# Kernel optimization log

Hardware: AMD Instinct MI355X
Metric: run time of the kernel (lower is better)

The kernel has to match this reference:

```python
import jax, jax.numpy as jnp
import numpy as np
import math

B, S, D, H, DF, L = 8, 1024, 1024, 16, 4096, 2
DK = D // H

def cosine_pe(seq_len, d_model):
    pos = jnp.arange(seq_len, dtype=jnp.float32)[:, None]
    div = jnp.exp(jnp.arange(0, d_model, 2, dtype=jnp.float32) * (-math.log(10000.0) / d_model))
    ang = pos * div[None, :]  # [S, D/2]
    # interleave sin (even cols) and cos (odd cols)
    return jnp.stack([jnp.sin(ang), jnp.cos(ang)], axis=-1).reshape(seq_len, d_model)

def layernorm(x, g, b, eps=1e-5):
    m = jnp.mean(x, axis=-1, keepdims=True)
    v = jnp.mean((x - m) ** 2, axis=-1, keepdims=True)
    return (x - m) / jnp.sqrt(v + eps) * g + b

def setup_inputs() -> dict:
    key = jax.random.key(0)
    ks = jax.random.split(key, 8)
    w = 0.03  # ~xavier scale for d_model=1024
    return {
        "q_embed_data": jax.random.normal(ks[0], (B, S, D), dtype=jnp.float32),
        "qa_embed_data": jax.random.normal(ks[1], (B, S, D), dtype=jnp.float32),
        "Wk": jax.random.normal(ks[2], (L, D, D), dtype=jnp.float32) * w,
        "bk": jnp.zeros((L, D), jnp.float32),
        "Wv": jax.random.normal(ks[3], (L, D, D), dtype=jnp.float32) * w,
        "bv": jnp.zeros((L, D), jnp.float32),
        "Wo": jax.random.normal(ks[4], (L, D, D), dtype=jnp.float32) * w,
        "bo": jnp.zeros((L, D), jnp.float32),
        "ln1_g": jnp.ones((L, D), jnp.float32),
        "ln1_b": jnp.zeros((L, D), jnp.float32),
        "W1": jax.random.normal(ks[5], (L, DF, D), dtype=jnp.float32) * w,
        "b1": jnp.zeros((L, DF), jnp.float32),
        "W2": jax.random.normal(ks[6], (L, D, DF), dtype=jnp.float32) * w,
        "b2": jnp.zeros((L, D), jnp.float32),
        "ln2_g": jnp.ones((L, D), jnp.float32),
        "ln2_b": jnp.zeros((L, D), jnp.float32),
    }

def reference(q_embed_data, qa_embed_data, Wk, bk, Wv, bv, Wo, bo, ln1_g, ln1_b, W1, b1, W2, b2, ln2_g, ln2_b):
    b, s, d = q_embed_data.shape
    pe = cosine_pe(s, d)
    x = q_embed_data + pe[None]   # query/key stream, updated per block
    y = qa_embed_data + pe[None]  # value stream, fixed across blocks
    idx = jnp.arange(s)
    allow = idx[None, :] < idx[:, None]  # strict causal: only past (j < i)
    n_blocks = Wk.shape[0]
    for l in range(n_blocks):
        # kq_same=True: q and k share k_linear
        q = (x @ Wk[l].T + bk[l]).reshape(b, s, H, DK).transpose(0, 2, 1, 3)
        k = q  # same input and same projection
        v = (y @ Wv[l].T + bv[l]).reshape(b, s, H, DK).transpose(0, 2, 1, 3)
        scores = jnp.einsum('bhid,bhjd->bhij', q, k) / math.sqrt(DK)
        scores = jnp.where(allow[None, None], scores, jnp.float32(-1e32))
        p = jax.nn.softmax(scores, axis=-1)
        p = p.at[:, :, 0, :].set(0.0)  # zero_pad first query row
        attn = jnp.einsum('bhij,bhjd->bhid', p, v).transpose(0, 2, 1, 3).reshape(b, s, d)
        attn = attn @ Wo[l].T + bo[l]
        x = layernorm(x + attn, ln1_g[l], ln1_b[l])
        ff = jax.nn.relu(x @ W1[l].T + b1[l]) @ W2[l].T + b2[l]
        x = layernorm(x + ff, ln2_g[l], ln2_b[l])
    return x
```

## Files before the change

### kernel.cpp

```cpp
#include <hip/hip_runtime.h>

using bf16   = __bf16;
using bf16x4 = __attribute__((ext_vector_type(4))) __bf16;
using bf16x8 = __attribute__((ext_vector_type(8))) __bf16;
using f32x4  = __attribute__((ext_vector_type(4))) float;

#define GLDS16(g, l)                                                            \
  __builtin_amdgcn_global_load_lds(                                             \
      (__attribute__((address_space(1))) void*)(g),                             \
      (__attribute__((address_space(3))) void*)(l), 16, 0, 0)

#define MFMA16(a, b, c) __builtin_amdgcn_mfma_f32_16x16x32_bf16(a, b, c, 0, 0, 0)

__device__ __forceinline__ int SW(int r, int s) {
  return r * 64 + (((s ^ (r & 7) ^ ((r >> 3) & 7)) & 7) << 3);
}

__device__ __forceinline__ float b2f(unsigned short u) {
  return (float)__builtin_bit_cast(bf16, u);
}

__device__ __forceinline__ bf16x8 scale8th(bf16x8 v) {
  bf16x8 r;
#pragma unroll
  for (int i = 0; i < 8; ++i) r[i] = (bf16)((float)v[i] * 0.125f);
  return r;
}

__global__ __launch_bounds__(256)
void init_pe(const float4* __restrict__ qd, const float4* __restrict__ qa,
             ushort4* __restrict__ xbf, ushort4* __restrict__ ybf) {
  const int n4 = 8 * 1024 * 1024 / 4;
  for (int i = blockIdx.x * 256 + threadIdx.x; i < n4; i += gridDim.x * 256) {
    int d4 = (i & 255) * 4;
    int ss = (i >> 8) & 1023;
    const float c = -0.0089944730195177f;
    float a0 = (float)ss * __expf((float)d4 * c);
    float a1 = (float)ss * __expf((float)(d4 + 2) * c);
    float p0 = sinf(a0), p1 = cosf(a0), p2 = sinf(a1), p3 = cosf(a1);
    float4 q4 = qd[i], y4 = qa[i];
    ushort4 xb, yb;
    xb.x = __builtin_bit_cast(unsigned short, (bf16)(q4.x + p0));
    xb.y = __builtin_bit_cast(unsigned short, (bf16)(q4.y + p1));
    xb.z = __builtin_bit_cast(unsigned short, (bf16)(q4.z + p2));
    xb.w = __builtin_bit_cast(unsigned short, (bf16)(q4.w + p3));
    yb.x = __builtin_bit_cast(unsigned short, (bf16)(y4.x + p0));
    yb.y = __builtin_bit_cast(unsigned short, (bf16)(y4.y + p1));
    yb.z = __builtin_bit_cast(unsigned short, (bf16)(y4.z + p2));
    yb.w = __builtin_bit_cast(unsigned short, (bf16)(y4.w + p3));
    xbf[i] = xb; ybf[i] = yb;
  }
}

__global__ __launch_bounds__(256)
void cvt5(const float4* __restrict__ s0, const float4* __restrict__ s1,
          const float4* __restrict__ s2, const float4* __restrict__ s3,
          const float4* __restrict__ s4,
          ushort4* __restrict__ dDD, ushort4* __restrict__ dDF,
          int n4dd, int n4df) {
  const int z = blockIdx.z;
  const float4* s = (z == 0) ? s0 : (z == 1) ? s1 : (z == 2) ? s2 : (z == 3) ? s3 : s4;
  ushort4* dd = (z < 3) ? dDD + (size_t)z * n4dd : dDF + (size_t)(z - 3) * n4df;
  const int n4 = (z < 3) ? n4dd : n4df;
  for (int i = blockIdx.x * 256 + threadIdx.x; i < n4; i += gridDim.x * 256) {
    float4 v = s[i];
    ushort4 o;
    o.x = __builtin_bit_cast(unsigned short, (bf16)v.x);
    o.y = __builtin_bit_cast(unsigned short, (bf16)v.y);
    o.z = __builtin_bit_cast(unsigned short, (bf16)v.z);
    o.w = __builtin_bit_cast(unsigned short, (bf16)v.w);
    dd[i] = o;
  }
}

template <int EPI, int MODE>
__global__ __launch_bounds__(256, 4)
void gemm_s(const bf16* __restrict__ A0, const bf16* __restrict__ W0,
            const float* __restrict__ b0, void* __restrict__ C0,
            const bf16* __restrict__ A1, const bf16* __restrict__ W1,
            const float* __restrict__ b1, void* __restrict__ C1,
            const int N, const int K) {
  __shared__ bf16 L[2][128 * 64];

  const int tid = threadIdx.x;
  const int wave = tid >> 6, lane = tid & 63;
  const int wm = wave >> 1, wn = wave & 1;
  const int cl = lane & 15, hk = lane >> 4;

  const int gx = gridDim.x;
  int flat = blockIdx.y * gx + blockIdx.x;
  flat = (flat & 7) * ((gx * gridDim.y) >> 3) + (flat >> 3);
  const int bcol = flat % gx, brow = flat / gx;
  const int z = (MODE == 0) ? 0 : blockIdx.z;

  const bf16* A = (MODE == 1 && z) ? A1 : A0;
  const bf16* W = (MODE == 1 && z) ? W1 : W0;
  const float* bias = (MODE == 1 && z) ? b1 : b0;
  void* C = (MODE == 1 && z) ? C1 : C0;

  const bf16* Ablk = A + (size_t)brow * 128 * K;
  const bf16* Wblk = W + (size_t)bcol * 128 * K;

  const int strow8 = lane >> 3;
  const int sl8 = (lane & 7) ^ (lane >> 3);

#define STAGE(kt)                                                               \
  do {                                                                          \
    _Pragma("unroll") for (int i_ = 0; i_ < 4; ++i_) {                          \
      int r0_ = i_ * 32 + wave * 8;                                             \
      GLDS16(Ablk + (size_t)(r0_ + strow8) * K + (size_t)(kt) * 64 + sl8 * 8,   \
             &L[0][r0_ * 64]);                                                  \
      GLDS16(Wblk + (size_t)(r0_ + strow8) * K + (size_t)(kt) * 64 + sl8 * 8,   \
             &L[1][r0_ * 64]);                                                  \
    }                                                                           \
  } while (0)

#define RD(reg, r_, kk_) \
  (*(const bf16x8*)&L[reg][(r_) * 64 + ((((kk_) * 4 + hk) ^ (cl & 7)) * 8)])

  f32x4 acc[4][4] = {};
  const int NT = K >> 6;

  for (int t = 0; t < NT; ++t) {
    STAGE(t);
    __syncthreads();
#pragma unroll
    for (int kk = 0; kk < 2; ++kk) {
      bf16x8 a4[4], b4[4];
#pragma unroll
      for (int m = 0; m < 4; ++m) a4[m] = RD(0, wm * 64 + m * 16 + cl, kk);
#pragma unroll
      for (int n = 0; n < 4; ++n) b4[n] = RD(1, wn * 64 + n * 16 + cl, kk);
      __builtin_amdgcn_s_setprio(1);
#pragma unroll
      for (int m = 0; m < 4; ++m)
#pragma unroll
        for (int n = 0; n < 4; ++n)
          acc[m][n] = MFMA16(a4[m], b4[n], acc[m][n]);
      __builtin_amdgcn_s_setprio(0);
    }
    __syncthreads();
  }
#undef STAGE
#undef RD

  float bv[4];
#pragma unroll
  for (int n = 0; n < 4; ++n)
    bv[n] = bias[bcol * 128 + wn * 64 + n * 16 + cl];

  const int crow0 = brow * 128 + wm * 64;
  const int ccol0 = bcol * 128 + wn * 64;
  char* esmem = (char*)(&L[0][0]) + wave * 4608;

  if (MODE == 1 && z == 1) {
    bf16* ep = (bf16*)esmem;
    const int h_ = ccol0 >> 6;
#pragma unroll
    for (int mp = 0; mp < 2; ++mp) {
#pragma unroll
      for (int mb = 0; mb < 2; ++mb) {
        int m = mp * 2 + mb;
#pragma unroll
        for (int n = 0; n < 4; ++n) {
          bf16x4 w4;
#pragma unroll
          for (int j = 0; j < 4; ++j) w4[j] = (bf16)(acc[m][n][j] + bv[n]);
          *(bf16x4*)&ep[(n * 16 + cl) * 36 + mb * 16 + hk * 4] = w4;
        }
      }
      asm volatile("s_waitcnt lgkmcnt(0)" ::: "memory");
      __builtin_amdgcn_sched_barrier(0);
      {
        const int t0 = crow0 + mp * 32;
        const int b_ = t0 >> 10, s_ = t0 & 1023;
        bf16* dst = (bf16*)C + ((size_t)(b_ * 16 + h_) * 64 + lane) * 1024 + s_;
        const bf16* src = &ep[lane * 36];
#pragma unroll
        for (int i = 0; i < 4; ++i)
          *(bf16x8*)&dst[i * 8] = *(const bf16x8*)&src[i * 8];
      }
      asm volatile("s_waitcnt lgkmcnt(0)" ::: "memory");
      __builtin_amdgcn_sched_barrier(0);
    }
  } else {
#pragma unroll
    for (int m = 0; m < 4; ++m) {
      bf16* ep = (bf16*)esmem;
#pragma unroll
      for (int n = 0; n < 4; ++n)
#pragma unroll
        for (int j = 0; j < 4; ++j) {
          float val = acc[m][n][j] + bv[n];
          if (EPI == 1) val = fmaxf(val, 0.f);
          ep[(hk * 4 + j) * 64 + n * 16 + cl] = (bf16)val;
        }
      asm volatile("s_waitcnt lgkmcnt(0)" ::: "memory");
      __builtin_amdgcn_sched_barrier(0);
#pragma unroll
      for (int i = 0; i < 2; ++i) {
        bf16x8 vv = ((const bf16x8*)ep)[lane + i * 64];
        const int row = crow0 + m * 16 + 8 * i + (lane >> 3);
        *(bf16x8*)((bf16*)C + (size_t)row * N + ccol0 + (lane & 7) * 8) = vv;
      }
      asm volatile("s_waitcnt lgkmcnt(0)" ::: "memory");
      __builtin_amdgcn_sched_barrier(0);
    }
  }
}

template <int EPI>
__global__ __launch_bounds__(512, 2)
void gemm8(const bf16* __restrict__ A, const bf16* __restrict__ W,
           const float* __restrict__ bias, bf16* __restrict__ C,
           const int N, const int K) {
  extern __shared__ bf16 lds[];

  const int tid = threadIdx.x;
  const int wave = tid >> 6, lane = tid & 63;
  const int wm = wave >> 2, wn = wave & 3;
  const int cl = lane & 15, hk = lane >> 4;
  const int sl8 = (lane & 7) ^ (lane >> 3);

  const int gx = gridDim.x;
  int flat = blockIdx.y * gx + blockIdx.x;
  flat = (flat & 7) * ((gx * gridDim.y) >> 3) + (flat >> 3);
  const int bcol = flat % gx, brow = flat / gx;

  const bf16* Ablk = A + (size_t)brow * 256 * K;
  const bf16* Wblk = W + (size_t)bcol * 256 * K;
  const size_t srow = (size_t)(wave * 8 + (lane >> 3)) * K + sl8 * 8;

  const int NT = K >> 6;

#define STG8(src, r0, dstbase, kt)                                             \
  do {                                                                         \
    _Pragma("unroll") for (int i_ = 0; i_ < 2; ++i_)                           \
      GLDS16((src) + srow + (size_t)((r0) + i_ * 64) * K + (size_t)(kt) * 64,  \
             (dstbase) + ((r0) + i_ * 64 + wave * 8) * 64);                    \
  } while (0)

#define RDF(base, r, kk) \
  (*(const bf16x8*)&(base)[(r) * 64 + ((((kk) * 4 + hk) ^ ((r) & 7)) * 8)])

#define BAR8 asm volatile("s_barrier" ::: "memory")

  STG8(Ablk, 0, lds, 0);
  STG8(Ablk, 128, lds, 0);
  STG8(Wblk, 0, lds + 16384, 0);
  STG8(Wblk, 128, lds + 16384, 0);
  STG8(Wblk, 0, lds + 49152, 1);
  STG8(Ablk, 0, lds + 32768, 1);
  asm volatile("s_waitcnt vmcnt(4)" ::: "memory");
  BAR8;

  f32x4 acc[2][2][4][2] = {};
  bf16x8 a[2][4], b0[2][2], b1[2][2];

  for (int t = 0; t < NT; ++t) {
    bf16* Ab = lds + (t & 1) * 32768;
    bf16* Bb = Ab + 16384;
    bf16* An = lds + (((t & 1) ^ 1)) * 32768;
    bf16* Bn = An + 16384;

#pragma unroll
    for (int kk = 0; kk < 2; ++kk) {
#pragma unroll
      for (int m_ = 0; m_ < 4; ++m_)
        a[kk][m_] = RDF(Ab, wm * 128 + m_ * 16 + cl, kk);
#pragma unroll
      for (int n_ = 0; n_ < 2; ++n_)
        b0[kk][n_] = RDF(Bb, wn * 64 + n_ * 16 + cl, kk);
    }
    if (t + 1 < NT) STG8(Ablk, 128, An, t + 1);
    BAR8;
    __builtin_amdgcn_s_setprio(1);
#pragma unroll
    for (int kk = 0; kk < 2; ++kk)
#pragma unroll
      for (int m_ = 0; m_ < 4; ++m_)
#pragma unroll
        for (int n_ = 0; n_ < 2; ++n_)
          acc[0][0][m_][n_] = MFMA16(a[kk][m_], b0[kk][n_], acc[0][0][m_][n_]);
    __builtin_amdgcn_s_setprio(0);
    BAR8;

#pragma unroll
    for (int kk = 0; kk < 2; ++kk)
#pragma unroll
      for (int n_ = 0; n_ < 2; ++n_)
        b1[kk][n_] = RDF(Bb, wn * 64 + 32 + n_ * 16 + cl, kk);
    if (t + 1 < NT) STG8(Wblk, 128, Bn, t + 1);
    BAR8;
    __builtin_amdgcn_s_setprio(1);
#pragma unroll
    for (int kk = 0; kk < 2; ++kk)
#pragma unroll
      for (int m_ = 0; m_ < 4; ++m_)
#pragma unroll
        for (int n_ = 0; n_ < 2; ++n_)
          acc[0][1][m_][n_] = MFMA16(a[kk][m_], b1[kk][n_], acc[0][1][m_][n_]);
    __builtin_amdgcn_s_setprio(0);
    BAR8;

#pragma unroll
    for (int kk = 0; kk < 2; ++kk)
#pragma unroll
      for (int m_ = 0; m_ < 4; ++m_)
        a[kk][m_] = RDF(Ab, wm * 128 + 64 + m_ * 16 + cl, kk);
    if (t + 2 < NT) STG8(Wblk, 0, Bb, t + 2);
    BAR8;
    __builtin_amdgcn_s_setprio(1);
#pragma unroll
    for (int kk = 0; kk < 2; ++kk)
#pragma unroll
      for (int m_ = 0; m_ < 4; ++m_)
#pragma unroll
        for (int n_ = 0; n_ < 2; ++n_)
          acc[1][0][m_][n_] = MFMA16(a[kk][m_], b0[kk][n_], acc[1][0][m_][n_]);
    __builtin_amdgcn_s_setprio(0);
    BAR8;

    if (t + 2 < NT) {
      STG8(Ablk, 0, Ab, t + 2);
      asm volatile("s_waitcnt vmcnt(4)" ::: "memory");
    } else if (t + 1 < NT) {
      asm volatile("s_waitcnt vmcnt(0)" ::: "memory");
    }
    BAR8;
    __builtin_amdgcn_s_setprio(1);
#pragma unroll
    for (int kk = 0; kk < 2; ++kk)
#pragma unroll
      for (int m_ = 0; m_ < 4; ++m_)
#pragma unroll
        for (int n_ = 0; n_ < 2; ++n_)
          acc[1][1][m_][n_] = MFMA16(a[kk][m_], b1[kk][n_], acc[1][1][m_][n_]);
    __builtin_amdgcn_s_setprio(0);
    BAR8;
  }
#undef STG8
#undef RDF
#undef BAR8

  __syncthreads();

  float bv[2][2];
#pragma unroll
  for (int nh = 0; nh < 2; ++nh)
#pragma unroll
    for (int n_ = 0; n_ < 2; ++n_)
      bv[nh][n_] = bias[bcol * 256 + wn * 64 + nh * 32 + n_ * 16 + cl];

  const int crow0 = brow * 256 + wm * 128;
  const int ccol0 = bcol * 256 + wn * 64;
  bf16* ep = lds + wave * 2304;

#pragma unroll
  for (int mh = 0; mh < 2; ++mh)
#pragma unroll
    for (int m_ = 0; m_ < 4; ++m_) {
#pragma unroll
      for (int nh = 0; nh < 2; ++nh)
#pragma unroll
        for (int n_ = 0; n_ < 2; ++n_)
#pragma unroll
          for (int j = 0; j < 4; ++j) {
            float val = acc[mh][nh][m_][n_][j] + bv[nh][n_];
            if (EPI == 1) val = fmaxf(val, 0.f);
            ep[(hk * 4 + j) * 64 + nh * 32 + n_ * 16 + cl] = (bf16)val;
          }
      asm volatile("s_waitcnt lgkmcnt(0)" ::: "memory");
      __builtin_amdgcn_sched_barrier(0);
#pragma unroll
      for (int i = 0; i < 2; ++i) {
        bf16x8 vv = ((const bf16x8*)ep)[lane + i * 64];
        const int row = crow0 + mh * 64 + m_ * 16 + 8 * i + (lane >> 3);
        *(bf16x8*)(C + (size_t)row * N + ccol0 + (lane & 7) * 8) = vv;
      }
      asm volatile("s_waitcnt lgkmcnt(0)" ::: "memory");
      __builtin_amdgcn_sched_barrier(0);
    }
}

#define SOFTMAX_PV(sc_, diag_, mreg, lreg, oacc)                                 \
  do {                                                                           \
    if (diag_) {                                                                 \
      _Pragma("unroll") for (int c = 0; c < 4; ++c)                              \
        _Pragma("unroll") for (int j = 0; j < 4; ++j)                            \
          if (c * 16 + hk * 4 + j >= wave * 16 + cl) sc_[c][j] = -1e30f;         \
    }                                                                            \
    float rl_[4];                                                                \
    _Pragma("unroll") for (int c = 0; c < 4; ++c)                                \
      rl_[c] = fmaxf(fmaxf(sc_[c][0], sc_[c][1]), fmaxf(sc_[c][2], sc_[c][3]));  \
    float rloc_ = fmaxf(fmaxf(rl_[0], rl_[1]), fmaxf(rl_[2], rl_[3]));           \
    if (!__all(rloc_ <= mreg)) {                                                 \
      float rmx_ = fmaxf(rloc_, __shfl_xor(rloc_, 16));                          \
      rmx_ = fmaxf(rmx_, __shfl_xor(rmx_, 32));                                  \
      float mn_ = fmaxf(mreg, rmx_);                                             \
      float sca_ = __expf(mreg - mn_);                                           \
      mreg = mn_;                                                                \
      lreg *= sca_;                                                              \
      float scr_[4];                                                             \
      _Pragma("unroll") for (int j = 0; j < 4; ++j)                              \
        scr_[j] = __shfl(sca_, hk * 4 + j);                                      \
      _Pragma("unroll") for (int c = 0; c < 4; ++c)                              \
        _Pragma("unroll") for (int j = 0; j < 4; ++j) oacc[c][j] *= scr_[j];     \
    }                                                                            \
    float ps_ = 0.f;                                                             \
    if (diag_) {                                                                 \
      _Pragma("unroll") for (int c = 0; c < 4; ++c) {                            \
        bf16x4 pk_;                                                              \
        _Pragma("unroll") for (int j = 0; j < 4; ++j) {                          \
          float e_ = (sc_[c][j] < -1e29f) ? 0.f : __expf(sc_[c][j] - mreg);      \
          ps_ += e_;                                                             \
          pk_[j] = (bf16)e_;                                                     \
        }                                                                        \
        *(bf16x4*)&Pw[SW(cl, c * 2 + (hk >> 1)) + (hk & 1) * 4] = pk_;           \
      }                                                                          \
    } else {                                                                     \
      _Pragma("unroll") for (int c = 0; c < 4; ++c) {                            \
        bf16x4 pk_;                                                              \
        _Pragma("unroll") for (int j = 0; j < 4; ++j) {                          \
          float e_ = __expf(sc_[c][j] - mreg);                                   \
          ps_ += e_;                                                             \
          pk_[j] = (bf16)e_;                                                     \
        }                                                                        \
        *(bf16x4*)&Pw[SW(cl, c * 2 + (hk >> 1)) + (hk & 1) * 4] = pk_;           \
      }                                                                          \
    }                                                                            \
    lreg += ps_;                  \
    const bf16x8 pa0_ = *(const bf16x8*)&Pw[SW(cl, hk)];                         \
    const bf16x8 pa1_ = *(const bf16x8*)&Pw[SW(cl, 4 + hk)];                     \
    __builtin_amdgcn_s_setprio(1);                                               \
    _Pragma("unroll") for (int c = 0; c < 4; ++c) {                              \
      const bf16x8 vf0_ = *(const bf16x8*)&Vb[SW(c * 16 + cl, hk)];              \
      const bf16x8 vf1_ = *(const bf16x8*)&Vb[SW(c * 16 + cl, 4 + hk)];          \
      oacc[c] = MFMA16(pa0_, vf0_, oacc[c]);                                     \
      oacc[c] = MFMA16(pa1_, vf1_, oacc[c]);                                     \
    }                                                                            \
    __builtin_amdgcn_s_setprio(0);                                               \
  } while (0)

__global__ __launch_bounds__(256, 2)
void attn_kernel(const bf16* __restrict__ q, const bf16* __restrict__ vT,
                 bf16* __restrict__ out) {
  const int S = 1024, D = 1024;
  const int f = blockIdx.y * 8 + blockIdx.x;
  const int g = f >> 3, xcd = f & 7;
  const int qa = g >> 4;
  const int bh = xcd * 16 + (g & 15);
  const int qb = 15 - qa;
  const int b = bh >> 4, h = bh & 15;
  const int tid = threadIdx.x, wave = tid >> 6, lane = tid & 63;

  __shared__ bf16 Ks[2][4096];
  __shared__ bf16 Vt[2][4096];
  __shared__ bf16 Ps[4][1024];

  const bf16* qp = q + (size_t)b * S * D + h * 64;
  const bf16* vp = vT + (size_t)(b * 16 + h) * 64 * 1024;

  const int cl = lane & 15;
  const int hk = lane >> 4;
  const int r0 = hk * 4;
  const int k8 = hk * 8;

  const int ksrow = lane >> 3;
  const int ksslot = (lane & 7) ^ (lane >> 3);

  const int rA = qa * 64 + wave * 16 + cl;
  const int rB = qb * 64 + wave * 16 + cl;
  const bf16x8 qA0 = scale8th(*(const bf16x8*)(qp + (size_t)rA * D + k8));
  const bf16x8 qA1 = scale8th(*(const bf16x8*)(qp + (size_t)rA * D + 32 + k8));
  const bf16x8 qB0 = scale8th(*(const bf16x8*)(qp + (size_t)rB * D + k8));
  const bf16x8 qB1 = scale8th(*(const bf16x8*)(qp + (size_t)rB * D + 32 + k8));

  f32x4 oA[4] = {}, oB[4] = {};
  float mA_ = -1e30f, lA_ = 0.f, mB_ = -1e30f, lB_ = 0.f;

  bf16* Pw = Ps[wave];
  int buf = 0;

#define STAGE_KV(dst_ks, dst_vt, jt_)                                            \
  do {                                                                           \
    _Pragma("unroll") for (int j = 0; j < 2; ++j) {                              \
      int ch = wave * 2 + j;                                                     \
      GLDS16(qp + (size_t)((jt_) * 64 + ch * 8 + ksrow) * D +                    \
                 ((ksslot ^ (ch & 7)) * 8),                                      \
             (dst_ks) + ch * 512);                                               \
      GLDS16(vp + (size_t)(ch * 8 + ksrow) * 1024 + (jt_) * 64 +                 \
                 ((ksslot ^ (ch & 7)) * 8),                                      \
             (dst_vt) + ch * 512);                                               \
    }                                                                            \
  } while (0)

  STAGE_KV(&Ks[0][0], &Vt[0][0], 0);
  __syncthreads();

  for (int jt = 0; jt <= qb; ++jt) {
    const int nxt = buf ^ 1;
    if (jt < qb) STAGE_KV(&Ks[nxt][0], &Vt[nxt][0], jt + 1);

    {
      const bf16* Kb = Ks[buf];
      const bf16* Vb = Vt[buf];
      const bool doA = (jt <= qa);
      const bool diagB = (jt == qb), diagA = (jt == qa);

      f32x4 scB[4], scA[4];
      __builtin_amdgcn_s_setprio(1);
#pragma unroll
      for (int c = 0; c < 4; ++c) {
        int r_ = c * 16 + cl;
        const bf16x8 kf0 = *(const bf16x8*)&Kb[SW(r_, hk)];
        const bf16x8 kf1 = *(const bf16x8*)&Kb[SW(r_, 4 + hk)];
        f32x4 zB = {};
        zB = MFMA16(kf0, qB0, zB);
        zB = MFMA16(kf1, qB1, zB);
        scB[c] = zB;
        if (doA) {
          f32x4 zA = {};
          zA = MFMA16(kf0, qA0, zA);
          zA = MFMA16(kf1, qA1, zA);
          scA[c] = zA;
        }
      }
      __builtin_amdgcn_s_setprio(0);

      SOFTMAX_PV(scB, diagB, mB_, lB_, oB);
      if (doA) SOFTMAX_PV(scA, diagA, mA_, lA_, oA);
    }
    __syncthreads();
    buf = nxt;
  }
#undef STAGE_KV

  lA_ += __shfl_xor(lA_, 16);
  lA_ += __shfl_xor(lA_, 32);
  lB_ += __shfl_xor(lB_, 16);
  lB_ += __shfl_xor(lB_, 32);

  bf16* ob = out + (size_t)b * S * D + h * 64;
  const float invA = (lA_ > 0.f) ? 1.f / lA_ : 0.f;
  const float invB = (lB_ > 0.f) ? 1.f / lB_ : 0.f;
#pragma unroll
  for (int j = 0; j < 4; ++j) {
    const float iA = __shfl(invA, hk * 4 + j);
    const float iB = __shfl(invB, hk * 4 + j);
    {
      int row = qa * 64 + wave * 16 + r0 + j;
#pragma unroll
      for (int c = 0; c < 4; ++c)
        ob[(size_t)row * D + c * 16 + cl] = (bf16)(oA[c][j] * iA);
    }
    {
      int row = qb * 64 + wave * 16 + r0 + j;
#pragma unroll
      for (int c = 0; c < 4; ++c)
        ob[(size_t)row * D + c * 16 + cl] = (bf16)(oB[c][j] * iB);
    }
  }
}

__global__ __launch_bounds__(256)
void add_ln(const ushort4* __restrict__ xin, const ushort4* __restrict__ y1b,
            const float* __restrict__ g, const float* __restrict__ bt,
            ushort4* __restrict__ xbf, float4* __restrict__ xout) {
  const int row = blockIdx.x;
  const int tid = threadIdx.x;
  const int wave = tid >> 6, lane = tid & 63;
  const size_t base4 = (size_t)row * 256 + tid;
  ushort4 a4 = xin[base4];
  ushort4 c4 = y1b[base4];
  float v0 = b2f(a4.x) + b2f(c4.x), v1 = b2f(a4.y) + b2f(c4.y);
  float v2 = b2f(a4.z) + b2f(c4.z), v3 = b2f(a4.w) + b2f(c4.w);

  float s = v0 + v1 + v2 + v3;
#pragma unroll
  for (int off = 32; off; off >>= 1) s += __shfl_xor(s, off);
  __shared__ float red1[4], red2[4];
  if (lane == 0) red1[wave] = s;
  __syncthreads();
  float mean = (red1[0] + red1[1] + red1[2] + red1[3]) * (1.f / 1024.f);

  float d0 = v0 - mean, d1 = v1 - mean, d2 = v2 - mean, d3 = v3 - mean;
  float vs = d0 * d0 + d1 * d1 + d2 * d2 + d3 * d3;
#pragma unroll
  for (int off = 32; off; off >>= 1) vs += __shfl_xor(vs, off);
  if (lane == 0) red2[wave] = vs;
  __syncthreads();
  float var = (red2[0] + red2[1] + red2[2] + red2[3]) * (1.f / 1024.f);
  float rstd = rsqrtf(var + 1e-5f);

  const int col = tid * 4;
  float4 gg = *(const float4*)(g + col);
  float4 bb = *(const float4*)(bt + col);
  float o0 = d0 * rstd * gg.x + bb.x;
  float o1 = d1 * rstd * gg.y + bb.y;
  float o2 = d2 * rstd * gg.z + bb.z;
  float o3 = d3 * rstd * gg.w + bb.w;
  if (xout) {
    float4 oo; oo.x = o0; oo.y = o1; oo.z = o2; oo.w = o3;
    xout[base4] = oo;
  } else {
    ushort4 ob;
    ob.x = __builtin_bit_cast(unsigned short, (bf16)o0);
    ob.y = __builtin_bit_cast(unsigned short, (bf16)o1);
    ob.z = __builtin_bit_cast(unsigned short, (bf16)o2);
    ob.w = __builtin_bit_cast(unsigned short, (bf16)o3);
    xbf[base4] = ob;
  }
}

extern "C" void kernel_launch(void* const* d_in, const int* in_sizes, int n_in,
                              void* d_out, int out_size, void* d_ws, size_t ws_size,
                              hipStream_t stream) {
  const float* qd  = (const float*)d_in[0];
  const float* qa  = (const float*)d_in[1];
  const float* Wk  = (const float*)d_in[2];
  const float* bk  = (const float*)d_in[3];
  const float* Wv  = (const float*)d_in[4];
  const float* bv  = (const float*)d_in[5];
  const float* Wo  = (const float*)d_in[6];
  const float* bo  = (const float*)d_in[7];
  const float* l1g = (const float*)d_in[8];
  const float* l1b = (const float*)d_in[9];
  const float* W1  = (const float*)d_in[10];
  const float* b1  = (const float*)d_in[11];
  const float* W2  = (const float*)d_in[12];
  const float* b2  = (const float*)d_in[13];
  const float* l2g = (const float*)d_in[14];
  const float* l2b = (const float*)d_in[15];

  const size_t DD = 1024 * 1024, DFD = 4096 * 1024, T = 8192;
  bf16* wkb = (bf16*)d_ws;
  bf16* wvb = wkb + 2 * DD;
  bf16* wob = wvb + 2 * DD;
  bf16* w1b = wob + 2 * DD;
  bf16* w2b = w1b + 2 * DFD;
  bf16* regA = w2b + 2 * DFD;
  bf16* qbf = regA;
  bf16* vbf = regA + 8388608;
  bf16* abf = regA + 16777216;
  bf16* ff1 = regA;
  bf16* xbf = regA + 33554432;
  bf16* ybf = xbf + 8388608;
  bf16* g1b = ybf + 8388608;

  static bool gemm8_attr = false;
  if (!gemm8_attr) {
    (void)hipFuncSetAttribute(reinterpret_cast<const void*>(&gemm8<1>),
                              hipFuncAttributeMaxDynamicSharedMemorySize, 131072);
    gemm8_attr = true;
  }

  init_pe<<<2048, 256, 0, stream>>>((const float4*)qd, (const float4*)qa,
                                    (ushort4*)xbf, (ushort4*)ybf);
  cvt5<<<dim3(1024, 1, 5), 256, 0, stream>>>(
      (const float4*)Wk, (const float4*)Wv, (const float4*)Wo,
      (const float4*)W1, (const float4*)W2,
      (ushort4*)wkb, (ushort4*)w1b, (int)(2 * DD / 4), (int)(2 * DFD / 4));

  for (int l = 0; l < 2; ++l) {
    gemm_s<0, 1><<<dim3(8, 64, 2), 256, 0, stream>>>(
        xbf, wkb + l * DD, bk + l * 1024, qbf,
        ybf, wvb + l * DD, bv + l * 1024, vbf, 1024, 1024);
    attn_kernel<<<dim3(8, 128), 256, 0, stream>>>(qbf, vbf, abf);
    gemm_s<0, 0><<<dim3(8, 64), 256, 0, stream>>>(
        abf, wob + l * DD, bo + l * 1024, g1b, nullptr, nullptr, nullptr, nullptr, 1024, 1024);
    add_ln<<<T, 256, 0, stream>>>((const ushort4*)xbf, (const ushort4*)g1b,
                                  l1g + l * 1024, l1b + l * 1024,
                                  (ushort4*)xbf, nullptr);
    gemm8<1><<<dim3(16, 32), 512, 131072, stream>>>(
        xbf, w1b + l * DFD, b1 + l * 4096, ff1, 4096, 1024);
    gemm_s<0, 0><<<dim3(8, 64), 256, 0, stream>>>(
        ff1, w2b + l * DFD, b2 + l * 1024, g1b, nullptr, nullptr, nullptr, nullptr, 1024, 4096);
    const bool last = (l == 1);
    add_ln<<<T, 256, 0, stream>>>((const ushort4*)xbf, (const ushort4*)g1b,
                                  l2g + l * 1024, l2b + l * 1024,
                                  (ushort4*)xbf, last ? (float4*)d_out : nullptr);
  }
  (void)in_sizes; (void)n_in; (void)out_size; (void)ws_size;
}
```

Measured before the change: 612.8 us.

## Restructure gemm8 pipeline with compile-time K and precomputed LDS offsets

Makes K a template parameter so the tile count is constexpr, and precomputes the swizzled LDS byte offsets for the A and B fragments so reads become base plus constant. It also reorders the global-to-LDS staging so that A and W for the next tile are issued earlier, and adds explicit lgkmcnt waits and sched barriers around each MFMA phase. The goal is less address arithmetic and better overlap of loads with MFMA work in the FFN1 GEMM. The reordered vmcnt bookkeeping is fragile: a wrong wait count could read stale LDS data.

```diff
diff --git a/kernel.cpp b/kernel.cpp
--- a/kernel.cpp
+++ b/kernel.cpp
@@ -209,17 +209,18 @@
   }
 }
 
-template <int EPI>
+template <int EPI, int K>
 __global__ __launch_bounds__(512, 2)
 void gemm8(const bf16* __restrict__ A, const bf16* __restrict__ W,
-           const float* __restrict__ bias, bf16* __restrict__ C,
-           const int N, const int K) {
+           const float* __restrict__ bias, bf16* __restrict__ C, const int N) {
   extern __shared__ bf16 lds[];
+  constexpr int NT = K >> 6;
 
   const int tid = threadIdx.x;
   const int wave = tid >> 6, lane = tid & 63;
   const int wm = wave >> 2, wn = wave & 3;
   const int cl = lane & 15, hk = lane >> 4;
+  const int c7 = cl & 7;
   const int sl8 = (lane & 7) ^ (lane >> 3);
 
   const int gx = gridDim.x;
@@ -227,52 +228,115 @@
   flat = (flat & 7) * ((gx * gridDim.y) >> 3) + (flat >> 3);
   const int bcol = flat % gx, brow = flat / gx;
 
-  const bf16* Ablk = A + (size_t)brow * 256 * K;
-  const bf16* Wblk = W + (size_t)bcol * 256 * K;
   const size_t srow = (size_t)(wave * 8 + (lane >> 3)) * K + sl8 * 8;
-
-  const int NT = K >> 6;
-
-#define STG8(src, r0, dstbase, kt)                                             \
+  const bf16* pA = A + (size_t)brow * 256 * K + srow;
+  const bf16* pW = W + (size_t)bcol * 256 * K + srow;
+  bf16* ldsw = lds + wave * 512;
+
+  int bA_[2][2], bB_[2][2];
+#pragma unroll
+  for (int b_ = 0; b_ < 2; ++b_)
+#pragma unroll
+    for (int kk = 0; kk < 2; ++kk) {
+      const int slot = ((kk * 4 + hk) ^ c7) * 16;
+      bA_[b_][kk] = b_ * 65536 + (wm * 128 + cl) * 128 + slot;
+      bB_[b_][kk] = b_ * 65536 + 32768 + (wn * 64 + cl) * 128 + slot;
+    }
+
+#define STG2(src, coff, roff, dstoff)                                          \
   do {                                                                         \
     _Pragma("unroll") for (int i_ = 0; i_ < 2; ++i_)                           \
-      GLDS16((src) + srow + (size_t)((r0) + i_ * 64) * K + (size_t)(kt) * 64,  \
-             (dstbase) + ((r0) + i_ * 64 + wave * 8) * 64);                    \
+      GLDS16((src) + (coff) + (size_t)((roff) + i_ * 64) * K,                  \
+             ldsw + (dstoff) + i_ * 4096);                                     \
   } while (0)
 
-#define RDF(base, r, kk) \
-  (*(const bf16x8*)&(base)[(r) * 64 + ((((kk) * 4 + hk) ^ ((r) & 7)) * 8)])
+#define LDA8(bf_, kk_, mh_, m_) \
+  (*(const bf16x8*)((const char*)lds + bA_[bf_][kk_] + (mh_)*8192 + (m_)*2048))
+#define LDB8(bf_, kk_, nh_, n_) \
+  (*(const bf16x8*)((const char*)lds + bB_[bf_][kk_] + (nh_)*4096 + (n_)*2048))
 
 #define BAR8 asm volatile("s_barrier" ::: "memory")
-
-  STG8(Ablk, 0, lds, 0);
-  STG8(Ablk, 128, lds, 0);
-  STG8(Wblk, 0, lds + 16384, 0);
-  STG8(Wblk, 128, lds + 16384, 0);
-  STG8(Wblk, 0, lds + 49152, 1);
-  STG8(Ablk, 0, lds + 32768, 1);
+#define LGKM0 do { asm volatile("s_waitcnt lgkmcnt(0)" ::: "memory"); \
+                   __builtin_amdgcn_sched_barrier(0); } while (0)
+
+  STG2(pA, 0, 0, 0);
+  STG2(pW, 0, 0, 16384);
+  STG2(pA, 0, 128, 8192);
+  STG2(pW, 0, 128, 16384 + 8192);
+  STG2(pW, 64, 0, 32768 + 16384);
+  STG2(pA, 64, 0, 32768);
   asm volatile("s_waitcnt vmcnt(4)" ::: "memory");
   BAR8;
 
   f32x4 acc[2][2][4][2] = {};
-  bf16x8 a[2][4], b0[2][2], b1[2][2];
-
+  bf16x8 af[2][4], b0f[2][2], b1f[2][2];
+
+#pragma unroll 2
   for (int t = 0; t < NT; ++t) {
-    bf16* Ab = lds + (t & 1) * 32768;
-    bf16* Bb = Ab + 16384;
-    bf16* An = lds + (((t & 1) ^ 1)) * 32768;
-    bf16* Bn = An + 16384;
+    const int bf_ = t & 1, nb_ = bf_ ^ 1;
+    const int co = t * 64;
 
 #pragma unroll
     for (int kk = 0; kk < 2; ++kk) {
 #pragma unroll
+      for (int m_ = 0; m_ < 4; ++m_) af[kk][m_] = LDA8(bf_, kk, 0, m_);
+#pragma unroll
+      for (int n_ = 0; n_ < 2; ++n_) b0f[kk][n_] = LDB8(bf_, kk, 0, n_);
+    }
+    if (t + 1 < NT) {
+      STG2(pA, co + 64, 128, nb_ * 32768 + 8192);
+      STG2(pW, co + 64, 128, nb_ * 32768 + 16384 + 8192);
+    }
+    asm volatile("s_waitcnt lgkmcnt(8)" ::: "memory");
+    BAR8;
+    LGKM0;
+    __builtin_amdgcn_s_setprio(1);
+#pragma unroll
+    for (int kk = 0; kk < 2; ++kk)
+#pragma unroll
       for (int m_ = 0; m_ < 4; ++m_)
-        a[kk][m_] = RDF(Ab, wm * 128 + m_ * 16 + cl, kk);
-#pragma unroll
-      for (int n_ = 0; n_ < 2; ++n_)
-        b0[kk][n_] = RDF(Bb, wn * 64 + n_ * 16 + cl, kk);
-    }
-    if (t + 1 < NT) STG8(Ablk, 128, An, t + 1);
+#pragma unroll
+        for (int n_ = 0; n_ < 2; ++n_)
+          acc[0][0][m_][n_] = MFMA16(af[kk][m_], b0f[kk][n_], acc[0][0][m_][n_]);
+    __builtin_amdgcn_s_setprio(0);
+    BAR8;
+
+#pragma unroll
+    for (int kk = 0; kk < 2; ++kk)
+#pragma unroll
+      for (int n_ = 0; n_ < 2; ++n_) b1f[kk][n_] = LDB8(bf_, kk, 1, n_);
+    BAR8;
+    LGKM0;
+    __builtin_amdgcn_s_setprio(1);
+#pragma unroll
+    for (int kk = 0; kk < 2; ++kk)
+#pragma unroll
+      for (int m_ = 0; m_ < 4; ++m_)
+#pragma unroll
+        for (int n_ = 0; n_ < 2; ++n_)
+          acc[0][1][m_][n_] = MFMA16(af[kk][m_], b1f[kk][n_], acc[0][1][m_][n_]);
+    __builtin_amdgcn_s_setprio(0);
+    BAR8;
+
+#pragma unroll
+    for (int kk = 0; kk < 2; ++kk)
+#pragma unroll
+      for (int m_ = 0; m_ < 4; ++m_) af[kk][m_] = LDA8(bf_, kk, 1, m_);
+    if (t + 2 < NT) STG2(pW, co + 128, 0, bf_ * 32768 + 16384);
+    BAR8;
+    LGKM0;
+    __builtin_amdgcn_s_setprio(1);
+#pragma unroll
+    for (int kk = 0; kk < 2; ++kk)
+#pragma unroll
+      for (int m_ = 0; m_ < 4; ++m_)
+#pragma unroll
+        for (int n_ = 0; n_ < 2; ++n_)
+          acc[1][0][m_][n_] = MFMA16(af[kk][m_], b0f[kk][n_], acc[1][0][m_][n_]);
+    __builtin_amdgcn_s_setprio(0);
+    BAR8;
+
+    if (t + 2 < NT) STG2(pA, co + 128, 0, bf_ * 32768);
     BAR8;
     __builtin_amdgcn_s_setprio(1);
 #pragma unroll
@@ -281,67 +345,20 @@
       for (int m_ = 0; m_ < 4; ++m_)
 #pragma unroll
         for (int n_ = 0; n_ < 2; ++n_)
-          acc[0][0][m_][n_] = MFMA16(a[kk][m_], b0[kk][n_], acc[0][0][m_][n_]);
+          acc[1][1][m_][n_] = MFMA16(af[kk][m_], b1f[kk][n_], acc[1][1][m_][n_]);
     __builtin_amdgcn_s_setprio(0);
+    if (t + 2 < NT) {
+      asm volatile("s_waitcnt vmcnt(4)" ::: "memory");
+    } else {
+      asm volatile("s_waitcnt vmcnt(0)" ::: "memory");
+    }
     BAR8;
-
-#pragma unroll
-    for (int kk = 0; kk < 2; ++kk)
-#pragma unroll
-      for (int n_ = 0; n_ < 2; ++n_)
-        b1[kk][n_] = RDF(Bb, wn * 64 + 32 + n_ * 16 + cl, kk);
-    if (t + 1 < NT) STG8(Wblk, 128, Bn, t + 1);
-    BAR8;
-    __builtin_amdgcn_s_setprio(1);
-#pragma unroll
-    for (int kk = 0; kk < 2; ++kk)
-#pragma unroll
-      for (int m_ = 0; m_ < 4; ++m_)
-#pragma unroll
-        for (int n_ = 0; n_ < 2; ++n_)
-          acc[0][1][m_][n_] = MFMA16(a[kk][m_], b1[kk][n_], acc[0][1][m_][n_]);
-    __builtin_amdgcn_s_setprio(0);
-    BAR8;
-
-#pragma unroll
-    for (int kk = 0; kk < 2; ++kk)
-#pragma unroll
-      for (int m_ = 0; m_ < 4; ++m_)
-        a[kk][m_] = RDF(Ab, wm * 128 + 64 + m_ * 16 + cl, kk);
-    if (t + 2 < NT) STG8(Wblk, 0, Bb, t + 2);
-    BAR8;
-    __builtin_amdgcn_s_setprio(1);
-#pragma unroll
-    for (int kk = 0; kk < 2; ++kk)
-#pragma unroll
-      for (int m_ = 0; m_ < 4; ++m_)
-#pragma unroll
-        for (int n_ = 0; n_ < 2; ++n_)
-          acc[1][0][m_][n_] = MFMA16(a[kk][m_], b0[kk][n_], acc[1][0][m_][n_]);
-    __builtin_amdgcn_s_setprio(0);
-    BAR8;
-
-    if (t + 2 < NT) {
-      STG8(Ablk, 0, Ab, t + 2);
-      asm volatile("s_waitcnt vmcnt(4)" ::: "memory");
-    } else if (t + 1 < NT) {
-      asm volatile("s_waitcnt vmcnt(0)" ::: "memory");
-    }
-    BAR8;
-    __builtin_amdgcn_s_setprio(1);
-#pragma unroll
-    for (int kk = 0; kk < 2; ++kk)
-#pragma unroll
-      for (int m_ = 0; m_ < 4; ++m_)
-#pragma unroll
-        for (int n_ = 0; n_ < 2; ++n_)
-          acc[1][1][m_][n_] = MFMA16(a[kk][m_], b1[kk][n_], acc[1][1][m_][n_]);
-    __builtin_amdgcn_s_setprio(0);
-    BAR8;
-  }
-#undef STG8
-#undef RDF
+  }
+#undef STG2
+#undef LDA8
+#undef LDB8
 #undef BAR8
+#undef LGKM0
 
   __syncthreads();
 
@@ -650,7 +667,7 @@
 
   static bool gemm8_attr = false;
   if (!gemm8_attr) {
-    (void)hipFuncSetAttribute(reinterpret_cast<const void*>(&gemm8<1>),
+    (void)hipFuncSetAttribute(reinterpret_cast<const void*>(&gemm8<1, 1024>),
                               hipFuncAttributeMaxDynamicSharedMemorySize, 131072);
     gemm8_attr = true;
   }
@@ -672,8 +689,8 @@
     add_ln<<<T, 256, 0, stream>>>((const ushort4*)xbf, (const ushort4*)g1b,
                                   l1g + l * 1024, l1b + l * 1024,
                                   (ushort4*)xbf, nullptr);
-    gemm8<1><<<dim3(16, 32), 512, 131072, stream>>>(
-        xbf, w1b + l * DFD, b1 + l * 4096, ff1, 4096, 1024);
+    gemm8<1, 1024><<<dim3(16, 32), 512, 131072, stream>>>(
+        xbf, w1b + l * DFD, b1 + l * 4096, ff1, 4096);
     gemm_s<0, 0><<<dim3(8, 64), 256, 0, stream>>>(
         ff1, w2b + l * DFD, b2 + l * 1024, g1b, nullptr, nullptr, nullptr, nullptr, 1024, 4096);
     const bool last = (l == 1);
```

Result: no change. 602.9 us (-1.6%).
